# Kernel tuning notes

Hardware: AMD Instinct MI355X
Metric: run time of the kernel (lower is better)

## Reference

```python
import jax, jax.numpy as jnp
import numpy as np

N = 50000          # atoms (nodes)
NEIGH = 12         # neighbors per atom
N_CRYS = 500       # crystals, 100 atoms each (contiguous)
H_E = 128          # h_fea_edge
H_A = 128          # h_fea_angle
N_CLS = 2
BOND_STEPS, BOND_MIN, BOND_MAX = 40, 0.0, 8.0
ANG_STEPS, ANG_MIN, ANG_MAX = 8, -1.0, 1.0


def _gbf(data, dmin, dmax, steps):
    # Gaussian basis expansion on the last (new) axis
    filters = jnp.linspace(dmin, dmax, steps, dtype=jnp.float32)
    gamma = (dmax - dmin) / steps
    return jnp.exp(-((data[..., None] - filters) ** 2) / (gamma ** 2))


def _sage_conv(x, src, dst, Wl, Wr, b):
    # PyG SAGEConv, mean aggregation:
    #   out_i = Wl @ mean_{(j->i) in E} x_j + b + Wr @ x_i
    n = x.shape[0]
    msg = x[src]                                             # [E, F] gather
    agg = jax.ops.segment_sum(msg, dst, num_segments=n)      # [N, F] scatter-add
    cnt = jax.ops.segment_sum(jnp.ones((src.shape[0],), x.dtype), dst, num_segments=n)
    agg = agg / jnp.maximum(cnt, 1.0)[:, None]
    return agg @ Wl.T + b + x @ Wr.T


def _segment_mean_pool(x, crys_idx):
    # crys_idx: [C, 2] contiguous [start, end) ranges covering [0, N)
    n = x.shape[0]
    starts = crys_idx[:, 0]
    seg_id = jnp.searchsorted(starts, jnp.arange(n), side='right') - 1
    counts = (crys_idx[:, 1] - crys_idx[:, 0]).astype(x.dtype)
    summed = jax.ops.segment_sum(x, seg_id, num_segments=crys_idx.shape[0])
    return summed / jnp.maximum(counts, 1.0)[:, None]


def setup_inputs() -> dict:
    key = jax.random.key(0)
    ks = jax.random.split(key, 24)
    in_b = BOND_STEPS * NEIGH            # 480
    in_a = ANG_STEPS * NEIGH * NEIGH     # 1152
    h_cat = H_E + H_A                    # 256

    def lin(k, fo, fi):
        return jax.random.normal(k, (fo, fi), jnp.float32) * (1.0 / np.sqrt(fi))

    atoms_per = N // N_CRYS
    starts = np.arange(N_CRYS, dtype=np.int32) * atoms_per
    crys_idx = jnp.asarray(np.stack([starts, starts + atoms_per], axis=1))

    return {
        'bond_fea': jax.random.uniform(ks[0], (N, NEIGH), jnp.float32) * BOND_MAX,
        'angle_fea': jax.random.uniform(ks[1], (N, NEIGH, NEIGH), jnp.float32) * 2.0 - 1.0,
        'species': jax.random.randint(ks[2], (N,), 0, 100, jnp.int32),
        'nbr_idx': jax.random.randint(ks[3], (N, NEIGH), 0, N, jnp.int32),
        'crys_idx': crys_idx,
        'Wl_b1': lin(ks[4], H_E, in_b), 'Wr_b1': lin(ks[5], H_E, in_b),
        'b_b1': jnp.zeros((H_E,), jnp.float32),
        'Wl_a1': lin(ks[6], H_A, in_a), 'Wr_a1': lin(ks[7], H_A, in_a),
        'b_a1': jnp.zeros((H_A,), jnp.float32),
        'Wl_b': jnp.stack([lin(ks[8], H_E, H_E), lin(ks[9], H_E, H_E)]),
        'Wr_b': jnp.stack([lin(ks[10], H_E, H_E), lin(ks[11], H_E, H_E)]),
        'b_b': jnp.zeros((2, H_E), jnp.float32),
        'Wl_a': jnp.stack([lin(ks[12], H_A, H_A), lin(ks[13], H_A, H_A)]),
        'Wr_a': jnp.stack([lin(ks[14], H_A, H_A), lin(ks[15], H_A, H_A)]),
        'b_a': jnp.zeros((2, H_A), jnp.float32),
        'W_mlp': jnp.stack([lin(ks[16], h_cat, h_cat), lin(ks[17], h_cat, h_cat)]),
        'b_mlp': jnp.zeros((2, h_cat), jnp.float32),
        'W_fc': lin(ks[18], N_CLS, h_cat),
        'b_fc': jnp.zeros((N_CLS,), jnp.float32),
    }


def reference(bond_fea, angle_fea, species, nbr_idx, crys_idx,
              Wl_b1, Wr_b1, b_b1, Wl_a1, Wr_a1, b_a1,
              Wl_b, Wr_b, b_b, Wl_a, Wr_a, b_a,
              W_mlp, b_mlp, W_fc, b_fc):
    n, neigh = nbr_idx.shape
    # get_edge_index: source = repeated node id, dest = neighbor id
    src = jnp.repeat(jnp.arange(n, dtype=nbr_idx.dtype), neigh)   # [N*neigh]
    dst = nbr_idx.reshape(-1)                                     # [N*neigh]

    # GBF expansions, flattened per node
    edge_fea = _gbf(bond_fea, BOND_MIN, BOND_MAX, BOND_STEPS).reshape(n, -1)    # [N, 480]
    ang_fea = _gbf(angle_fea, ANG_MIN, ANG_MAX, ANG_STEPS).reshape(n, -1)       # [N, 1152]

    # first SAGE layers (dropout_prob = 0 -> identity)
    b_out = jax.nn.relu(_sage_conv(edge_fea, src, dst, Wl_b1, Wr_b1, b_b1))
    a_out = jax.nn.relu(_sage_conv(ang_fea, src, dst, Wl_a1, Wr_a1, b_a1))

    # stacked SAGE layers (n_conv - 1 = 2 each)
    for i in range(Wl_b.shape[0]):
        b_out = jax.nn.relu(_sage_conv(b_out, src, dst, Wl_b[i], Wr_b[i], b_b[i]))
    for i in range(Wl_a.shape[0]):
        a_out = jax.nn.relu(_sage_conv(a_out, src, dst, Wl_a[i], Wr_a[i], b_a[i]))

    crys_fea = jnp.concatenate([b_out, a_out], axis=1)   # [N, 256]
    crys_fea = _segment_mean_pool(crys_fea, crys_idx)     # [C, 256]

    for i in range(W_mlp.shape[0]):
        crys_fea = crys_fea @ W_mlp[i].T + b_mlp[i]

    return crys_fea @ W_fc.T + b_fc                       # [C, n_classification]
```

## Files before the change

### kernel.cpp

```cpp
#include <hip/hip_runtime.h>

typedef _Float16 f16;
typedef _Float16 f16x8 __attribute__((ext_vector_type(8)));
typedef float f32x4 __attribute__((ext_vector_type(4)));

#define N_ATOMS 50000
#define NEIGH   12
#define NEDGE   (N_ATOMS * NEIGH)
#define NCRYS   500
#define NBLK    196

template <int C>
__global__ __launch_bounds__(256) void transposeT(const float* __restrict__ in,
                                                  float* __restrict__ outp) {
  __shared__ float tile[64 * C];
  const int r0 = blockIdx.x * 64;
  const int nr = min(64, N_ATOMS - r0);
  for (int idx = threadIdx.x; idx < nr * C; idx += 256) {
    int r = idx / C, c = idx - r * C;
    tile[r * C + c] = in[(size_t)(r0 + r) * C + c];
  }
  __syncthreads();
  for (int idx = threadIdx.x; idx < 64 * C; idx += 256) {
    int c = idx >> 6, r = idx & 63;
    if (r < nr) outp[(size_t)c * N_ATOMS + r0 + r] = tile[r * C + c];
  }
}

template <int MODE, int K>
__global__ __launch_bounds__(256) void gemm1_reg(
    const float* __restrict__ AT, const f16* __restrict__ Wcat,
    f16* __restrict__ P, f16* __restrict__ Q, int n) {
  const int lane = threadIdx.x & 63;
  const int wid = threadIdx.x >> 6;
  const int wr = wid & 1;
  const int wc = wid >> 1;
  const int row0 = blockIdx.x * 128;
  const f16* Wh = Wcat + (size_t)blockIdx.y * 128 * K;
  f16* outp = blockIdx.y ? Q : P;
  const int r16 = lane & 15;
  const int kb = lane >> 4;

  int rm[4];
#pragma unroll
  for (int m = 0; m < 4; ++m) {
    int r = row0 + wr * 64 + m * 16 + r16;
    rm[m] = (r < n) ? r : (n - 1);
  }
  const f16* wb[4];
#pragma unroll
  for (int q = 0; q < 4; ++q)
    wb[q] = Wh + (size_t)(wc * 64 + q * 16 + r16) * K + kb * 8;

  f32x4 acc[4][4];
#pragma unroll
  for (int m = 0; m < 4; ++m)
#pragma unroll
    for (int q = 0; q < 4; ++q) acc[m][q] = (f32x4)0.f;

  constexpr int NT = K / 32;
  float d0[4];
  f16x8 b0[4];
  {
    int kg = kb * 8;
    int jn = (MODE == 1) ? kg / 40 : (kg >> 3);
#pragma unroll
    for (int m = 0; m < 4; ++m) d0[m] = AT[(size_t)jn * N_ATOMS + rm[m]];
#pragma unroll
    for (int q = 0; q < 4; ++q) b0[q] = *(const f16x8*)(wb[q]);
  }

  for (int t = 0; t < NT; ++t) {
    float d1[4];
    f16x8 b1[4];
    if (t + 1 < NT) {
      int kg = (t + 1) * 32 + kb * 8;
      int jn = (MODE == 1) ? kg / 40 : (kg >> 3);
#pragma unroll
      for (int m = 0; m < 4; ++m) d1[m] = AT[(size_t)jn * N_ATOMS + rm[m]];
#pragma unroll
      for (int q = 0; q < 4; ++q) b1[q] = *(const f16x8*)(wb[q] + (t + 1) * 32);
    }
    f16x8 a[4];
    float fbase, fstep, g2i;
    if constexpr (MODE == 1) {
      int kg = t * 32 + kb * 8;
      int jn = kg / 40;
      fbase = (float)(kg - jn * 40) * (8.0f / 39.0f);
      fstep = 8.0f / 39.0f;
      g2i = 25.0f;
    } else {
      fbase = -1.0f;
      fstep = 2.0f / 7.0f;
      g2i = 16.0f;
    }
#pragma unroll
    for (int m = 0; m < 4; ++m) {
      float dd = d0[m];
#pragma unroll
      for (int j = 0; j < 8; ++j) {
        float tt = dd - (fbase + (float)j * fstep);
        a[m][j] = (f16)__expf(-tt * tt * g2i);
      }
    }
#pragma unroll
    for (int m = 0; m < 4; ++m)
#pragma unroll
      for (int q = 0; q < 4; ++q)
        acc[m][q] =
            __builtin_amdgcn_mfma_f32_16x16x32_f16(a[m], b0[q], acc[m][q], 0, 0, 0);
#pragma unroll
    for (int m = 0; m < 4; ++m) d0[m] = d1[m];
#pragma unroll
    for (int q = 0; q < 4; ++q) b0[q] = b1[q];
  }

  const int crow = (lane >> 4) * 4;
  const int ccol = lane & 15;
#pragma unroll
  for (int m = 0; m < 4; ++m) {
#pragma unroll
    for (int r = 0; r < 4; ++r) {
      int row = row0 + wr * 64 + m * 16 + crow + r;
      if (row < n) {
#pragma unroll
        for (int q = 0; q < 4; ++q)
          outp[(size_t)row * 128 + wc * 64 + q * 16 + ccol] = (f16)acc[m][q][r];
      }
    }
  }
}

__global__ __launch_bounds__(256) void gemmL_reg(
    const f16* __restrict__ srcB, const f16* __restrict__ srcA,
    f16* __restrict__ dstB, f16* __restrict__ dstA, const f16* __restrict__ Wall,
    const float* __restrict__ bb, const float* __restrict__ ba, int lidx, int n) {
  const int path = blockIdx.y;
  const f16* src = path ? srcA : srcB;
  f16* dst = path ? dstA : dstB;
  const f16* W = Wall + (size_t)(path * 2 + lidx) * 32768;
  const float* bias = (path ? ba : bb) + lidx * 128;

  const int lane = threadIdx.x & 63;
  const int wid = threadIdx.x >> 6;
  const int wr = wid & 1;
  const int wc = wid >> 1;
  const int row0 = blockIdx.x * 128;
  const int r16 = lane & 15;
  const int kb = lane >> 4;

  int rm[4];
#pragma unroll
  for (int m = 0; m < 4; ++m) {
    int r = row0 + wr * 64 + m * 16 + r16;
    rm[m] = (r < n) ? r : (n - 1);
  }
  const f16* wb[4];
#pragma unroll
  for (int q = 0; q < 4; ++q)
    wb[q] = W + (size_t)(wc * 64 + q * 16 + r16) * 256 + kb * 8;

  f32x4 acc[4][4];
#pragma unroll
  for (int m = 0; m < 4; ++m)
#pragma unroll
    for (int q = 0; q < 4; ++q) acc[m][q] = (f32x4)0.f;

  f16x8 a0[4], b0[4];
#pragma unroll
  for (int m = 0; m < 4; ++m)
    a0[m] = *(const f16x8*)&src[(size_t)rm[m] * 256 + kb * 8];
#pragma unroll
  for (int q = 0; q < 4; ++q) b0[q] = *(const f16x8*)(wb[q]);

  for (int t = 0; t < 8; ++t) {
    f16x8 a1[4], b1[4];
    if (t + 1 < 8) {
      int k = (t + 1) * 32 + kb * 8;
#pragma unroll
      for (int m = 0; m < 4; ++m)
        a1[m] = *(const f16x8*)&src[(size_t)rm[m] * 256 + k];
#pragma unroll
      for (int q = 0; q < 4; ++q) b1[q] = *(const f16x8*)(wb[q] + (t + 1) * 32);
    }
#pragma unroll
    for (int m = 0; m < 4; ++m)
#pragma unroll
      for (int q = 0; q < 4; ++q)
        acc[m][q] =
            __builtin_amdgcn_mfma_f32_16x16x32_f16(a0[m], b0[q], acc[m][q], 0, 0, 0);
#pragma unroll
    for (int m = 0; m < 4; ++m) a0[m] = a1[m];
#pragma unroll
    for (int q = 0; q < 4; ++q) b0[q] = b1[q];
  }

  const int crow = (lane >> 4) * 4;
  const int ccol = lane & 15;
#pragma unroll
  for (int m = 0; m < 4; ++m) {
#pragma unroll
    for (int r = 0; r < 4; ++r) {
      int row = row0 + wr * 64 + m * 16 + crow + r;
      if (row < n) {
#pragma unroll
        for (int q = 0; q < 4; ++q) {
          int col = wc * 64 + q * 16 + ccol;
          float v = acc[m][q][r] + bias[col];
          dst[(size_t)row * 256 + 128 + col] = (f16)fmaxf(v, 0.0f);
        }
      }
    }
  }
}

__global__ void cvtW(const float* __restrict__ Wl, const float* __restrict__ Wr,
                     f16* __restrict__ outp, int K) {
  int c = blockIdx.y;
  int k = blockIdx.x * 256 + threadIdx.x;
  if (k < K)
    outp[(size_t)c * K + k] =
        (f16)((c < 128) ? Wl[(size_t)c * K + k] : Wr[(size_t)(c - 128) * K + k]);
}

__global__ void cvtW_small(const float* __restrict__ Wl_b, const float* __restrict__ Wr_b,
                           const float* __restrict__ Wl_a, const float* __restrict__ Wr_a,
                           f16* __restrict__ outp) {
  int idx = blockIdx.x * 256 + threadIdx.x;
  int l = idx >> 15;
  int c = (idx >> 8) & 127;
  int k = idx & 255;
  const float* Wl = (l < 2) ? Wl_b + (size_t)l * 16384 : Wl_a + (size_t)(l - 2) * 16384;
  const float* Wr = (l < 2) ? Wr_b + (size_t)l * 16384 : Wr_a + (size_t)(l - 2) * 16384;
  float v = (k < 128) ? Wl[(size_t)c * 128 + k] : Wr[(size_t)c * 128 + (k - 128)];
  outp[idx] = (f16)v;
}

__global__ void k_count(const int* __restrict__ nbr, int* __restrict__ deg) {
  int e = blockIdx.x * 256 + threadIdx.x;
  if (e < NEDGE) atomicAdd(&deg[nbr[e]], 1);
}
__global__ void k_scan1(const int* __restrict__ deg, int* __restrict__ rowptr,
                        int* __restrict__ bsum) {
  __shared__ int s[256];
  int t = threadIdx.x, i = blockIdx.x * 256 + t;
  int v = (i < N_ATOMS) ? deg[i] : 0;
  s[t] = v;
  __syncthreads();
  for (int off = 1; off < 256; off <<= 1) {
    int x = (t >= off) ? s[t - off] : 0;
    __syncthreads();
    s[t] += x;
    __syncthreads();
  }
  if (i < N_ATOMS) rowptr[i] = s[t] - v;
  if (t == 255) bsum[blockIdx.x] = s[255];
}
__global__ void k_scan2(int* __restrict__ bsum) {
  __shared__ int s[256];
  int t = threadIdx.x;
  int v = (t < NBLK) ? bsum[t] : 0;
  s[t] = v;
  __syncthreads();
  for (int off = 1; off < 256; off <<= 1) {
    int x = (t >= off) ? s[t - off] : 0;
    __syncthreads();
    s[t] += x;
    __syncthreads();
  }
  if (t < NBLK) bsum[t] = s[t] - v;
}
__global__ void k_scan3(int* __restrict__ rowptr, const int* __restrict__ bsum) {
  int i = blockIdx.x * 256 + threadIdx.x;
  if (i < N_ATOMS) rowptr[i] += bsum[blockIdx.x];
  if (i == 0) rowptr[N_ATOMS] = NEDGE;
}
__global__ void k_fill(const int* __restrict__ nbr, const int* __restrict__ rowptr,
                       int* __restrict__ cursor, int* __restrict__ eidx) {
  int e = blockIdx.x * 256 + threadIdx.x;
  if (e < NEDGE) {
    int dst = nbr[e];
    int pos = rowptr[dst] + atomicAdd(&cursor[dst], 1);
    eidx[pos] = e / NEIGH;
  }
}

__global__ __launch_bounds__(256) void gather_fin1(
    const f16* __restrict__ Pb, const f16* __restrict__ Qb,
    const f16* __restrict__ Pa, const f16* __restrict__ Qa,
    const int* __restrict__ rowptr, const int* __restrict__ eidx,
    const float* __restrict__ bias_b, const float* __restrict__ bias_a,
    f16* __restrict__ axb, f16* __restrict__ axa) {
  const int path = blockIdx.y;
  const f16* P = path ? Pa : Pb;
  const f16* Q = path ? Qa : Qb;
  const float* bias = path ? bias_a : bias_b;
  f16* ax = path ? axa : axb;
  const int t = threadIdx.x;
  const int a = blockIdx.x * 16 + (t >> 4);
  const int g = (t & 15) * 8;
  const int s0 = rowptr[a], s1 = rowptr[a + 1];
  float acc[8];
#pragma unroll
  for (int u = 0; u < 8; ++u) acc[u] = 0.f;
  int j = s0;
  for (; j + 4 <= s1; j += 4) {
    int src0 = eidx[j], src1 = eidx[j + 1], src2 = eidx[j + 2], src3 = eidx[j + 3];
    f16x8 v0 = *(const f16x8*)&P[(size_t)src0 * 128 + g];
    f16x8 v1 = *(const f16x8*)&P[(size_t)src1 * 128 + g];
    f16x8 v2 = *(const f16x8*)&P[(size_t)src2 * 128 + g];
    f16x8 v3 = *(const f16x8*)&P[(size_t)src3 * 128 + g];
#pragma unroll
    for (int u = 0; u < 8; ++u)
      acc[u] += ((float)v0[u] + (float)v1[u]) + ((float)v2[u] + (float)v3[u]);
  }
  for (; j < s1; ++j) {
    f16x8 v = *(const f16x8*)&P[(size_t)eidx[j] * 128 + g];
#pragma unroll
    for (int u = 0; u < 8; ++u) acc[u] += (float)v[u];
  }
  f16x8 q = *(const f16x8*)&Q[(size_t)a * 128 + g];
  float inv = 1.0f / fmaxf((float)(s1 - s0), 1.0f);
  f16 outv[8];
#pragma unroll
  for (int u = 0; u < 8; ++u) {
    float v = acc[u] * inv + bias[g + u] + (float)q[u];
    outv[u] = (f16)fmaxf(v, 0.0f);
  }
  *(f16x8*)&ax[(size_t)a * 256 + 128 + g] = *(const f16x8*)outv;
}

__global__ __launch_bounds__(256) void gather_mean(
    f16* __restrict__ axb, f16* __restrict__ axa,
    const int* __restrict__ rowptr, const int* __restrict__ eidx) {
  f16* ax = blockIdx.y ? axa : axb;
  const int t = threadIdx.x;
  const int a = blockIdx.x * 16 + (t >> 4);
  const int g = (t & 15) * 8;
  const int s0 = rowptr[a], s1 = rowptr[a + 1];
  float acc[8];
#pragma unroll
  for (int u = 0; u < 8; ++u) acc[u] = 0.f;
  int j = s0;
  for (; j + 4 <= s1; j += 4) {
    int src0 = eidx[j], src1 = eidx[j + 1], src2 = eidx[j + 2], src3 = eidx[j + 3];
    f16x8 v0 = *(const f16x8*)&ax[(size_t)src0 * 256 + 128 + g];
    f16x8 v1 = *(const f16x8*)&ax[(size_t)src1 * 256 + 128 + g];
    f16x8 v2 = *(const f16x8*)&ax[(size_t)src2 * 256 + 128 + g];
    f16x8 v3 = *(const f16x8*)&ax[(size_t)src3 * 256 + 128 + g];
#pragma unroll
    for (int u = 0; u < 8; ++u)
      acc[u] += ((float)v0[u] + (float)v1[u]) + ((float)v2[u] + (float)v3[u]);
  }
  for (; j < s1; ++j) {
    f16x8 v = *(const f16x8*)&ax[(size_t)eidx[j] * 256 + 128 + g];
#pragma unroll
    for (int u = 0; u < 8; ++u) acc[u] += (float)v[u];
  }
  float inv = 1.0f / fmaxf((float)(s1 - s0), 1.0f);
  f16 outv[8];
#pragma unroll
  for (int u = 0; u < 8; ++u) outv[u] = (f16)(acc[u] * inv);
  *(f16x8*)&ax[(size_t)a * 256 + g] = *(const f16x8*)outv;
}

__global__ __launch_bounds__(256) void head_kernel(
    const f16* __restrict__ axb, const f16* __restrict__ axa,
    const int* __restrict__ crys, const float* __restrict__ W_mlp,
    const float* __restrict__ b_mlp, const float* __restrict__ W_fc,
    const float* __restrict__ b_fc, float* __restrict__ outp) {
  __shared__ float sh0[256], sh1[256];
  const int cry = blockIdx.x, c = threadIdx.x;
  const int s = crys[2 * cry], e = crys[2 * cry + 1];
  const f16* src = (c < 128) ? axb : axa;
  const int ch = c & 127;
  float sum = 0.f;
  for (int r = s; r < e; ++r) sum += (float)src[(size_t)r * 256 + 128 + ch];
  sh0[c] = sum / fmaxf((float)(e - s), 1.0f);
  __syncthreads();
  {
    const float* wrow = W_mlp + (size_t)c * 256;
    float s2 = b_mlp[c];
#pragma unroll 8
    for (int k = 0; k < 256; k += 4) {
      float4 w = *(const float4*)&wrow[k];
      s2 += sh0[k] * w.x + sh0[k + 1] * w.y + sh0[k + 2] * w.z + sh0[k + 3] * w.w;
    }
    sh1[c] = s2;
  }
  __syncthreads();
  {
    const float* wrow = W_mlp + 65536 + (size_t)c * 256;
    float s2 = b_mlp[256 + c];
#pragma unroll 8
    for (int k = 0; k < 256; k += 4) {
      float4 w = *(const float4*)&wrow[k];
      s2 += sh1[k] * w.x + sh1[k + 1] * w.y + sh1[k + 2] * w.z + sh1[k + 3] * w.w;
    }
    sh0[c] = s2;
  }
  __syncthreads();
  if (c < 2) {
    const float* wrow = W_fc + c * 256;
    float s2 = b_fc[c];
    for (int k = 0; k < 256; ++k) s2 += sh0[k] * wrow[k];
    outp[cry * 2 + c] = s2;
  }
}

extern "C" void kernel_launch(void* const* d_in, const int* in_sizes, int n_in,
                              void* d_out, int out_size, void* d_ws, size_t ws_size,
                              hipStream_t stream) {
  const float* bond  = (const float*)d_in[0];
  const float* angle = (const float*)d_in[1];
  const int*   nbr   = (const int*)d_in[3];
  const int*   crys  = (const int*)d_in[4];
  const float* Wl_b1 = (const float*)d_in[5];
  const float* Wr_b1 = (const float*)d_in[6];
  const float* b_b1  = (const float*)d_in[7];
  const float* Wl_a1 = (const float*)d_in[8];
  const float* Wr_a1 = (const float*)d_in[9];
  const float* b_a1  = (const float*)d_in[10];
  const float* Wl_b  = (const float*)d_in[11];
  const float* Wr_b  = (const float*)d_in[12];
  const float* b_b   = (const float*)d_in[13];
  const float* Wl_a  = (const float*)d_in[14];
  const float* Wr_a  = (const float*)d_in[15];
  const float* b_a   = (const float*)d_in[16];
  const float* W_mlp = (const float*)d_in[17];
  const float* b_mlp = (const float*)d_in[18];
  const float* W_fc  = (const float*)d_in[19];
  const float* b_fc  = (const float*)d_in[20];

  char* w = (char*)d_ws;
  auto alloc = [&](size_t bytes) {
    void* p = (void*)w;
    w += (bytes + 255) & ~(size_t)255;
    return p;
  };
  f16* axbA = (f16*)alloc((size_t)N_ATOMS * 256 * 2);
  f16* axaA = (f16*)alloc((size_t)N_ATOMS * 256 * 2);
  f16* axbB = (f16*)alloc((size_t)N_ATOMS * 256 * 2);
  f16* axaB = (f16*)alloc((size_t)N_ATOMS * 256 * 2);
  f16* Pb = axbB;
  f16* Qb = axbB + (size_t)N_ATOMS * 128;
  f16* Pa = axaB;
  f16* Qa = axaB + (size_t)N_ATOMS * 128;
  float* angleT = (float*)alloc((size_t)144 * N_ATOMS * 4);
  float* bondT  = (float*)alloc((size_t)12 * N_ATOMS * 4);
  f16* Wb1c = (f16*)alloc((size_t)256 * 480 * 2);
  f16* Wa1c = (f16*)alloc((size_t)256 * 1152 * 2);
  f16* Wsm  = (f16*)alloc((size_t)4 * 128 * 256 * 2);
  int* deg    = (int*)alloc((size_t)2 * N_ATOMS * 4);
  int* cursor = deg + N_ATOMS;
  int* rowptr = (int*)alloc((size_t)(N_ATOMS + 1) * 4);
  int* eidx   = (int*)alloc((size_t)NEDGE * 4);
  int* bsum   = (int*)alloc(256 * 4);

  const int TT = (N_ATOMS + 63) / 64;

  transposeT<144><<<TT, 256, 0, stream>>>(angle, angleT);
  transposeT<12><<<TT, 256, 0, stream>>>(bond, bondT);

  cvtW<<<dim3(2, 256), 256, 0, stream>>>(Wl_b1, Wr_b1, Wb1c, 480);
  cvtW<<<dim3(5, 256), 256, 0, stream>>>(Wl_a1, Wr_a1, Wa1c, 1152);
  cvtW_small<<<512, 256, 0, stream>>>(Wl_b, Wr_b, Wl_a, Wr_a, Wsm);

  hipMemsetAsync(deg, 0, (size_t)2 * N_ATOMS * 4, stream);
  k_count<<<(NEDGE + 255) / 256, 256, 0, stream>>>(nbr, deg);
  k_scan1<<<NBLK, 256, 0, stream>>>(deg, rowptr, bsum);
  k_scan2<<<1, 256, 0, stream>>>(bsum);
  k_scan3<<<NBLK, 256, 0, stream>>>(rowptr, bsum);
  k_fill<<<(NEDGE + 255) / 256, 256, 0, stream>>>(nbr, rowptr, cursor, eidx);

  const int GG = (N_ATOMS + 127) / 128;
  const int AG = N_ATOMS / 16;

  gemm1_reg<2, 1152><<<dim3(GG, 2), 256, 0, stream>>>(angleT, Wa1c, Pa, Qa, N_ATOMS);
  gemm1_reg<1, 480><<<dim3(GG, 2), 256, 0, stream>>>(bondT, Wb1c, Pb, Qb, N_ATOMS);
  gather_fin1<<<dim3(AG, 2), 256, 0, stream>>>(Pb, Qb, Pa, Qa, rowptr, eidx,
                                               b_b1, b_a1, axbA, axaA);

  gather_mean<<<dim3(AG, 2), 256, 0, stream>>>(axbA, axaA, rowptr, eidx);
  gemmL_reg<<<dim3(GG, 2), 256, 0, stream>>>(axbA, axaA, axbB, axaB, Wsm, b_b, b_a,
                                             0, N_ATOMS);
  gather_mean<<<dim3(AG, 2), 256, 0, stream>>>(axbB, axaB, rowptr, eidx);
  gemmL_reg<<<dim3(GG, 2), 256, 0, stream>>>(axbB, axaB, axbA, axaA, Wsm, b_b, b_a,
                                             1, N_ATOMS);

  head_kernel<<<NCRYS, 256, 0, stream>>>(axbA, axaA, crys, W_mlp, b_mlp, W_fc, b_fc,
                                         (float*)d_out);
}
```

Measured before the change: 479.1 us.

## Fuse GBF expansion into shared-memory staged first-layer GEMM, drop transposes

The first-layer GEMM now reads bond and angle features directly in row-major layout, builds the Gaussian basis once per block into double-buffered LDS, and covers both output halves (P and Q) in one 512-thread block. The exponentials use a recurrence (successive ratio multiplies) instead of one exp per entry. This removes the two transpose kernels and the duplicated exp work across the former two y-blocks. It adds block-level syncs and f16 rounding from the recurrence. The small GEMM drops manual prefetch in favor of full unrolling, and the gather loops process 8 neighbors per iteration for more memory-level parallelism.

```diff
diff --git a/kernel.cpp b/kernel.cpp
--- a/kernel.cpp
+++ b/kernel.cpp
@@ -10,47 +10,36 @@
 #define NCRYS   500
 #define NBLK    196
 
-template <int C>
-__global__ __launch_bounds__(256) void transposeT(const float* __restrict__ in,
-                                                  float* __restrict__ outp) {
-  __shared__ float tile[64 * C];
-  const int r0 = blockIdx.x * 64;
-  const int nr = min(64, N_ATOMS - r0);
-  for (int idx = threadIdx.x; idx < nr * C; idx += 256) {
-    int r = idx / C, c = idx - r * C;
-    tile[r * C + c] = in[(size_t)(r0 + r) * C + c];
-  }
-  __syncthreads();
-  for (int idx = threadIdx.x; idx < 64 * C; idx += 256) {
-    int c = idx >> 6, r = idx & 63;
-    if (r < nr) outp[(size_t)c * N_ATOMS + r0 + r] = tile[r * C + c];
-  }
-}
-
 template <int MODE, int K>
-__global__ __launch_bounds__(256) void gemm1_reg(
-    const float* __restrict__ AT, const f16* __restrict__ Wcat,
+__global__ __launch_bounds__(512) void gemm1(
+    const float* __restrict__ Asrc, const f16* __restrict__ Wcat,
     f16* __restrict__ P, f16* __restrict__ Q, int n) {
-  const int lane = threadIdx.x & 63;
-  const int wid = threadIdx.x >> 6;
-  const int wr = wid & 1;
-  const int wc = wid >> 1;
+  __shared__ __align__(16) f16 As[2][4][128][8];
+  const int tid = threadIdx.x;
+  const int lane = tid & 63;
+  const int wid = tid >> 6;
+  const int wr = wid >> 2;
+  const int wc = wid & 3;
   const int row0 = blockIdx.x * 128;
-  const f16* Wh = Wcat + (size_t)blockIdx.y * 128 * K;
-  f16* outp = blockIdx.y ? Q : P;
   const int r16 = lane & 15;
   const int kb = lane >> 4;
 
-  int rm[4];
-#pragma unroll
-  for (int m = 0; m < 4; ++m) {
-    int r = row0 + wr * 64 + m * 16 + r16;
-    rm[m] = (r < n) ? r : (n - 1);
-  }
+  const int sAkb = tid & 3;
+  const int sArow = tid >> 2;
+  int arow = row0 + sArow;
+  if (arow >= n) arow = n - 1;
+
   const f16* wb[4];
 #pragma unroll
   for (int q = 0; q < 4; ++q)
-    wb[q] = Wh + (size_t)(wc * 64 + q * 16 + r16) * K + kb * 8;
+    wb[q] = Wcat + (size_t)(wc * 64 + q * 16 + r16) * K + kb * 8;
+
+  constexpr float G2I = (MODE == 1) ? 25.0f : 16.0f;
+  constexpr float DLT = (MODE == 1) ? (8.0f / 39.0f) : (2.0f / 7.0f);
+  constexpr float C1 = 2.0f * G2I * DLT;
+  constexpr float C2 = G2I * DLT * DLT;
+  const float S = __expf(-2.0f * C2);
+  constexpr int RUN = (MODE == 1) ? 4 : 8;
 
   f32x4 acc[4][4];
 #pragma unroll
@@ -58,65 +47,68 @@
 #pragma unroll
     for (int q = 0; q < 4; ++q) acc[m][q] = (f32x4)0.f;
 
+  auto stageA = [&](int buf, int t) {
+    int kg0 = t * 32 + sAkb * 8;
+    int jn, kk0;
+    if constexpr (MODE == 1) {
+      jn = kg0 / 40;
+      kk0 = kg0 - jn * 40;
+    } else {
+      jn = kg0 >> 3;
+      kk0 = 0;
+    }
+    float d = Asrc[(size_t)arow * (MODE == 1 ? 12 : 144) + jn];
+    f16 v[8];
+#pragma unroll
+    for (int h = 0; h < 8 / RUN; ++h) {
+      float f0 = (float)(kk0 + h * RUN) * DLT + (MODE == 2 ? -1.0f : 0.0f);
+      float u = d - f0;
+      float g = __expf(-G2I * u * u);
+      float ratio = __expf(C1 * u - C2);
+      v[h * RUN] = (f16)g;
+#pragma unroll
+      for (int j = 1; j < RUN; ++j) {
+        g *= ratio;
+        ratio *= S;
+        v[h * RUN + j] = (f16)g;
+      }
+    }
+    *(f16x8*)&As[buf][sAkb][sArow][0] = *(const f16x8*)v;
+  };
+
   constexpr int NT = K / 32;
-  float d0[4];
-  f16x8 b0[4];
-  {
-    int kg = kb * 8;
-    int jn = (MODE == 1) ? kg / 40 : (kg >> 3);
-#pragma unroll
-    for (int m = 0; m < 4; ++m) d0[m] = AT[(size_t)jn * N_ATOMS + rm[m]];
-#pragma unroll
-    for (int q = 0; q < 4; ++q) b0[q] = *(const f16x8*)(wb[q]);
-  }
-
+  f16x8 bcur[4], bnxt[4];
+  stageA(0, 0);
+#pragma unroll
+  for (int q = 0; q < 4; ++q) bcur[q] = *(const f16x8*)(wb[q]);
+  __syncthreads();
+  int buf = 0;
   for (int t = 0; t < NT; ++t) {
-    float d1[4];
-    f16x8 b1[4];
     if (t + 1 < NT) {
-      int kg = (t + 1) * 32 + kb * 8;
-      int jn = (MODE == 1) ? kg / 40 : (kg >> 3);
-#pragma unroll
-      for (int m = 0; m < 4; ++m) d1[m] = AT[(size_t)jn * N_ATOMS + rm[m]];
-#pragma unroll
-      for (int q = 0; q < 4; ++q) b1[q] = *(const f16x8*)(wb[q] + (t + 1) * 32);
+      stageA(buf ^ 1, t + 1);
+#pragma unroll
+      for (int q = 0; q < 4; ++q) bnxt[q] = *(const f16x8*)(wb[q] + (t + 1) * 32);
     }
     f16x8 a[4];
-    float fbase, fstep, g2i;
-    if constexpr (MODE == 1) {
-      int kg = t * 32 + kb * 8;
-      int jn = kg / 40;
-      fbase = (float)(kg - jn * 40) * (8.0f / 39.0f);
-      fstep = 8.0f / 39.0f;
-      g2i = 25.0f;
-    } else {
-      fbase = -1.0f;
-      fstep = 2.0f / 7.0f;
-      g2i = 16.0f;
-    }
-#pragma unroll
-    for (int m = 0; m < 4; ++m) {
-      float dd = d0[m];
-#pragma unroll
-      for (int j = 0; j < 8; ++j) {
-        float tt = dd - (fbase + (float)j * fstep);
-        a[m][j] = (f16)__expf(-tt * tt * g2i);
-      }
-    }
+#pragma unroll
+    for (int m = 0; m < 4; ++m)
+      a[m] = *(const f16x8*)&As[buf][kb][wr * 64 + m * 16 + r16][0];
 #pragma unroll
     for (int m = 0; m < 4; ++m)
 #pragma unroll
       for (int q = 0; q < 4; ++q)
         acc[m][q] =
-            __builtin_amdgcn_mfma_f32_16x16x32_f16(a[m], b0[q], acc[m][q], 0, 0, 0);
-#pragma unroll
-    for (int m = 0; m < 4; ++m) d0[m] = d1[m];
-#pragma unroll
-    for (int q = 0; q < 4; ++q) b0[q] = b1[q];
+            __builtin_amdgcn_mfma_f32_16x16x32_f16(a[m], bcur[q], acc[m][q], 0, 0, 0);
+    __syncthreads();
+#pragma unroll
+    for (int q = 0; q < 4; ++q) bcur[q] = bnxt[q];
+    buf ^= 1;
   }
 
   const int crow = (lane >> 4) * 4;
   const int ccol = lane & 15;
+  f16* outp = (wc < 2) ? P : Q;
+  const int cbase = (wc & 1) * 64;
 #pragma unroll
   for (int m = 0; m < 4; ++m) {
 #pragma unroll
@@ -125,7 +117,7 @@
       if (row < n) {
 #pragma unroll
         for (int q = 0; q < 4; ++q)
-          outp[(size_t)row * 128 + wc * 64 + q * 16 + ccol] = (f16)acc[m][q][r];
+          outp[(size_t)row * 128 + cbase + q * 16 + ccol] = (f16)acc[m][q][r];
       }
     }
   }
@@ -166,33 +158,20 @@
 #pragma unroll
     for (int q = 0; q < 4; ++q) acc[m][q] = (f32x4)0.f;
 
-  f16x8 a0[4], b0[4];
-#pragma unroll
-  for (int m = 0; m < 4; ++m)
-    a0[m] = *(const f16x8*)&src[(size_t)rm[m] * 256 + kb * 8];
-#pragma unroll
-  for (int q = 0; q < 4; ++q) b0[q] = *(const f16x8*)(wb[q]);
-
+#pragma unroll
   for (int t = 0; t < 8; ++t) {
-    f16x8 a1[4], b1[4];
-    if (t + 1 < 8) {
-      int k = (t + 1) * 32 + kb * 8;
-#pragma unroll
-      for (int m = 0; m < 4; ++m)
-        a1[m] = *(const f16x8*)&src[(size_t)rm[m] * 256 + k];
-#pragma unroll
-      for (int q = 0; q < 4; ++q) b1[q] = *(const f16x8*)(wb[q] + (t + 1) * 32);
-    }
+    f16x8 a[4], b[4];
+#pragma unroll
+    for (int m = 0; m < 4; ++m)
+      a[m] = *(const f16x8*)&src[(size_t)rm[m] * 256 + t * 32 + kb * 8];
+#pragma unroll
+    for (int q = 0; q < 4; ++q) b[q] = *(const f16x8*)(wb[q] + t * 32);
 #pragma unroll
     for (int m = 0; m < 4; ++m)
 #pragma unroll
       for (int q = 0; q < 4; ++q)
         acc[m][q] =
-            __builtin_amdgcn_mfma_f32_16x16x32_f16(a0[m], b0[q], acc[m][q], 0, 0, 0);
-#pragma unroll
-    for (int m = 0; m < 4; ++m) a0[m] = a1[m];
-#pragma unroll
-    for (int q = 0; q < 4; ++q) b0[q] = b1[q];
+            __builtin_amdgcn_mfma_f32_16x16x32_f16(a[m], b[q], acc[m][q], 0, 0, 0);
   }
 
   const int crow = (lane >> 4) * 4;
@@ -304,20 +283,32 @@
 #pragma unroll
   for (int u = 0; u < 8; ++u) acc[u] = 0.f;
   int j = s0;
+  for (; j + 8 <= s1; j += 8) {
+    int e[8];
+#pragma unroll
+    for (int u = 0; u < 8; ++u) e[u] = eidx[j + u];
+    f16x8 v[8];
+#pragma unroll
+    for (int u = 0; u < 8; ++u) v[u] = *(const f16x8*)&P[(size_t)e[u] * 128 + g];
+#pragma unroll
+    for (int u = 0; u < 8; ++u)
+#pragma unroll
+      for (int c = 0; c < 8; ++c) acc[c] += (float)v[u][c];
+  }
   for (; j + 4 <= s1; j += 4) {
-    int src0 = eidx[j], src1 = eidx[j + 1], src2 = eidx[j + 2], src3 = eidx[j + 3];
-    f16x8 v0 = *(const f16x8*)&P[(size_t)src0 * 128 + g];
-    f16x8 v1 = *(const f16x8*)&P[(size_t)src1 * 128 + g];
-    f16x8 v2 = *(const f16x8*)&P[(size_t)src2 * 128 + g];
-    f16x8 v3 = *(const f16x8*)&P[(size_t)src3 * 128 + g];
-#pragma unroll
-    for (int u = 0; u < 8; ++u)
-      acc[u] += ((float)v0[u] + (float)v1[u]) + ((float)v2[u] + (float)v3[u]);
+    int e0 = eidx[j], e1 = eidx[j + 1], e2 = eidx[j + 2], e3 = eidx[j + 3];
+    f16x8 v0 = *(const f16x8*)&P[(size_t)e0 * 128 + g];
+    f16x8 v1 = *(const f16x8*)&P[(size_t)e1 * 128 + g];
+    f16x8 v2 = *(const f16x8*)&P[(size_t)e2 * 128 + g];
+    f16x8 v3 = *(const f16x8*)&P[(size_t)e3 * 128 + g];
+#pragma unroll
+    for (int c = 0; c < 8; ++c)
+      acc[c] += ((float)v0[c] + (float)v1[c]) + ((float)v2[c] + (float)v3[c]);
   }
   for (; j < s1; ++j) {
     f16x8 v = *(const f16x8*)&P[(size_t)eidx[j] * 128 + g];
 #pragma unroll
-    for (int u = 0; u < 8; ++u) acc[u] += (float)v[u];
+    for (int c = 0; c < 8; ++c) acc[c] += (float)v[c];
   }
   f16x8 q = *(const f16x8*)&Q[(size_t)a * 128 + g];
   float inv = 1.0f / fmaxf((float)(s1 - s0), 1.0f);
@@ -342,20 +333,33 @@
 #pragma unroll
   for (int u = 0; u < 8; ++u) acc[u] = 0.f;
   int j = s0;
+  for (; j + 8 <= s1; j += 8) {
+    int e[8];
+#pragma unroll
+    for (int u = 0; u < 8; ++u) e[u] = eidx[j + u];
+    f16x8 v[8];
+#pragma unroll
+    for (int u = 0; u < 8; ++u)
+      v[u] = *(const f16x8*)&ax[(size_t)e[u] * 256 + 128 + g];
+#pragma unroll
+    for (int u = 0; u < 8; ++u)
+#pragma unroll
+      for (int c = 0; c < 8; ++c) acc[c] += (float)v[u][c];
+  }
   for (; j + 4 <= s1; j += 4) {
-    int src0 = eidx[j], src1 = eidx[j + 1], src2 = eidx[j + 2], src3 = eidx[j + 3];
-    f16x8 v0 = *(const f16x8*)&ax[(size_t)src0 * 256 + 128 + g];
-    f16x8 v1 = *(const f16x8*)&ax[(size_t)src1 * 256 + 128 + g];
-    f16x8 v2 = *(const f16x8*)&ax[(size_t)src2 * 256 + 128 + g];
-    f16x8 v3 = *(const f16x8*)&ax[(size_t)src3 * 256 + 128 + g];
-#pragma unroll
-    for (int u = 0; u < 8; ++u)
-      acc[u] += ((float)v0[u] + (float)v1[u]) + ((float)v2[u] + (float)v3[u]);
+    int e0 = eidx[j], e1 = eidx[j + 1], e2 = eidx[j + 2], e3 = eidx[j + 3];
+    f16x8 v0 = *(const f16x8*)&ax[(size_t)e0 * 256 + 128 + g];
+    f16x8 v1 = *(const f16x8*)&ax[(size_t)e1 * 256 + 128 + g];
+    f16x8 v2 = *(const f16x8*)&ax[(size_t)e2 * 256 + 128 + g];
+    f16x8 v3 = *(const f16x8*)&ax[(size_t)e3 * 256 + 128 + g];
+#pragma unroll
+    for (int c = 0; c < 8; ++c)
+      acc[c] += ((float)v0[c] + (float)v1[c]) + ((float)v2[c] + (float)v3[c]);
   }
   for (; j < s1; ++j) {
     f16x8 v = *(const f16x8*)&ax[(size_t)eidx[j] * 256 + 128 + g];
 #pragma unroll
-    for (int u = 0; u < 8; ++u) acc[u] += (float)v[u];
+    for (int c = 0; c < 8; ++c) acc[c] += (float)v[c];
   }
   float inv = 1.0f / fmaxf((float)(s1 - s0), 1.0f);
   f16 outv[8];
@@ -446,8 +450,6 @@
   f16* Qb = axbB + (size_t)N_ATOMS * 128;
   f16* Pa = axaB;
   f16* Qa = axaB + (size_t)N_ATOMS * 128;
-  float* angleT = (float*)alloc((size_t)144 * N_ATOMS * 4);
-  float* bondT  = (float*)alloc((size_t)12 * N_ATOMS * 4);
   f16* Wb1c = (f16*)alloc((size_t)256 * 480 * 2);
   f16* Wa1c = (f16*)alloc((size_t)256 * 1152 * 2);
   f16* Wsm  = (f16*)alloc((size_t)4 * 128 * 256 * 2);
@@ -457,11 +459,6 @@
   int* eidx   = (int*)alloc((size_t)NEDGE * 4);
   int* bsum   = (int*)alloc(256 * 4);
 
-  const int TT = (N_ATOMS + 63) / 64;
-
-  transposeT<144><<<TT, 256, 0, stream>>>(angle, angleT);
-  transposeT<12><<<TT, 256, 0, stream>>>(bond, bondT);
-
   cvtW<<<dim3(2, 256), 256, 0, stream>>>(Wl_b1, Wr_b1, Wb1c, 480);
   cvtW<<<dim3(5, 256), 256, 0, stream>>>(Wl_a1, Wr_a1, Wa1c, 1152);
   cvtW_small<<<512, 256, 0, stream>>>(Wl_b, Wr_b, Wl_a, Wr_a, Wsm);
@@ -476,8 +473,8 @@
   const int GG = (N_ATOMS + 127) / 128;
   const int AG = N_ATOMS / 16;
 
-  gemm1_reg<2, 1152><<<dim3(GG, 2), 256, 0, stream>>>(angleT, Wa1c, Pa, Qa, N_ATOMS);
-  gemm1_reg<1, 480><<<dim3(GG, 2), 256, 0, stream>>>(bondT, Wb1c, Pb, Qb, N_ATOMS);
+  gemm1<2, 1152><<<GG, 512, 0, stream>>>(angle, Wa1c, Pa, Qa, N_ATOMS);
+  gemm1<1, 480><<<GG, 512, 0, stream>>>(bond, Wb1c, Pb, Qb, N_ATOMS);
   gather_fin1<<<dim3(AG, 2), 256, 0, stream>>>(Pb, Qb, Pa, Qa, rowptr, eidx,
                                                b_b1, b_a1, axbA, axaA);
 
```

Result: faster. 451.8 us (-5.7%).
